# Optimization experiments

Hardware: AMD Instinct MI355X
Metric: run time of the kernel (lower is better)

## Reference

```python
import jax, jax.numpy as jnp
import numpy as np

N = 100000
EPS = 1e-5

def gcn_conv(x, W, b, src, dst, n):
    # linear transform first (PyG GCNConv): [N, H]
    h = x @ W
    # add self-loops
    loop = jnp.arange(n, dtype=src.dtype)
    s = jnp.concatenate([src, loop])
    d = jnp.concatenate([dst, loop])
    # symmetric normalization deg^{-1/2}[s] * deg^{-1/2}[d]
    deg = jax.ops.segment_sum(jnp.ones_like(d, dtype=h.dtype), d, num_segments=n)
    dinv = jnp.where(deg > 0, jax.lax.rsqrt(jnp.maximum(deg, 1.0) * 0 + jnp.where(deg > 0, deg, 1.0)), 0.0)
    norm = dinv[s] * dinv[d]
    msg = h[s] * norm[:, None]          # gather + scale: [E+N, H]
    out = jax.ops.segment_sum(msg, d, num_segments=n)  # scatter-add
    return out + b

def batch_norm(x, gamma, beta):
    mu = jnp.mean(x, axis=0)
    var = jnp.mean((x - mu) ** 2, axis=0)  # biased var, as BatchNorm1d training
    return (x - mu) * jax.lax.rsqrt(var + EPS) * gamma + beta

def setup_inputs() -> dict:
    key = jax.random.key(0)
    ks = jax.random.split(key, 8)
    D, H, O = 64, 64, 32
    E = 1600000
    x = jax.random.normal(ks[0], (N, D), dtype=jnp.float32)
    edge_index = jax.random.randint(ks[1], (2, E), 0, N, dtype=jnp.int64)
    W1 = jax.random.normal(ks[2], (D, H), dtype=jnp.float32) / np.sqrt(D)
    b1 = jnp.zeros((H,), dtype=jnp.float32)
    W2 = jax.random.normal(ks[3], (H, H), dtype=jnp.float32) / np.sqrt(H)
    b2 = jnp.zeros((H,), dtype=jnp.float32)
    gamma1 = jnp.ones((H,), dtype=jnp.float32); beta1 = jnp.zeros((H,), dtype=jnp.float32)
    gamma2 = jnp.ones((H,), dtype=jnp.float32); beta2 = jnp.zeros((H,), dtype=jnp.float32)
    Wfc = jax.random.normal(ks[4], (H, O), dtype=jnp.float32) / np.sqrt(H)
    bfc = jnp.zeros((O,), dtype=jnp.float32)
    return {"x": x, "edge_index": edge_index, "W1": W1, "b1": b1, "gamma1": gamma1, "beta1": beta1,
            "W2": W2, "b2": b2, "gamma2": gamma2, "beta2": beta2, "Wfc": Wfc, "bfc": bfc}

def reference(x, edge_index, W1, b1, gamma1, beta1, W2, b2, gamma2, beta2, Wfc, bfc):
    src, dst = edge_index[0], edge_index[1]
    h = jax.nn.relu(gcn_conv(x, W1, b1, src, dst, N))
    h = batch_norm(h, gamma1, beta1)
    h = jax.nn.relu(gcn_conv(h, W2, b2, src, dst, N))
    h = batch_norm(h, gamma2, beta2)
    return h @ Wfc + bfc
```

## Files before the change

kernel.cpp:

```cpp
#include <hip/hip_runtime.h>
#include <hip/hip_bf16.h>
#include <cstdint>
#include <cstddef>

#define NBK 128
#define BKB 512

static __device__ __forceinline__ unsigned pack_bf16(float a, float b) {
  __hip_bfloat16 lo = __float2bfloat16(a), hi = __float2bfloat16(b);
  unsigned short ulo = *reinterpret_cast<unsigned short*>(&lo);
  unsigned short uhi = *reinterpret_cast<unsigned short*>(&hi);
  return ((unsigned)uhi << 16) | ulo;
}
static __device__ __forceinline__ float blo(unsigned u) {
  union { unsigned q; float f; } x; x.q = u << 16; return x.f;
}
static __device__ __forceinline__ float bhi(unsigned u) {
  union { unsigned q; float f; } x; x.q = u & 0xffff0000u; return x.f;
}


__launch_bounds__(256)
__global__ void bucket_kernel(const int* __restrict__ src, const int* __restrict__ dst,
                              int E, int cap, int nbk,
                              int* __restrict__ bcur, int* __restrict__ rcnt,
                              int* __restrict__ bkt_d, int* __restrict__ bkt_s) {
  __shared__ int cnt[NBK], base[NBK], gbase[NBK], curb[NBK], pbase[NBK];
  __shared__ int ptot_s;
  __shared__ int stg_d[3200], stg_s[3200];
  int t = threadIdx.x;
  int chunk = (E + BKB - 1) / BKB;
  int ebeg = blockIdx.x * chunk;
  int eend = min(E, ebeg + chunk);
  int nloc = eend - ebeg;
  for (int q = t; q < nbk; q += 256) { cnt[q] = 0; curb[q] = 0; }
  __syncthreads();

  int dl[13], sl[13];
  int nr = (nloc + 255) >> 8;
#pragma unroll 13
  for (int u = 0; u < nr; ++u) {
    int li = (u << 8) + t;
    bool v = li < nloc;
    int i = ebeg + (v ? li : 0);
    int d = v ? __builtin_nontemporal_load(&dst[i]) : 0;
    int s = v ? __builtin_nontemporal_load(&src[i]) : 0;
    dl[u] = d; sl[u] = s;
    if (v) atomicAdd(&cnt[d >> 10], 1);
  }
  __syncthreads();
  if (t == 0) {
    int run = 0, prun = 0;
    for (int q = 0; q < nbk; ++q) {
      base[q] = run;  run += cnt[q];
      pbase[q] = prun; prun += (cnt[q] + 15) & ~15;
    }
    ptot_s = prun;
  }
  __syncthreads();
  for (int q = t; q < nbk; q += 256) {
    int c = cnt[q];
    if (c > 0) {
      gbase[q] = atomicAdd(&bcur[q], (c + 15) & ~15);
      atomicAdd(&rcnt[q], c);
    } else gbase[q] = 0;
  }
#pragma unroll 13
  for (int u = 0; u < nr; ++u) {
    int li = (u << 8) + t;
    if (li < nloc) {
      int b = dl[u] >> 10;
      int pos = atomicAdd(&curb[b], 1) + base[b];
      stg_d[pos] = dl[u]; stg_s[pos] = sl[u];
    }
  }
  __syncthreads();
  int ptot = ptot_s;
  for (int i = t; i < ptot; i += 256) {
    int lo = 0, hi = nbk - 1;
    while (lo < hi) {
      int mid = (lo + hi + 1) >> 1;
      if (pbase[mid] <= i) lo = mid; else hi = mid - 1;
    }
    int q = lo;
    int j = i - pbase[q];
    int dv = -1, sv = 0;
    if (j < cnt[q]) { dv = stg_d[base[q] + j]; sv = stg_s[base[q] + j]; }
    size_t o = (size_t)q * cap + gbase[q] + j;
    bkt_d[o] = dv;
    bkt_s[o] = sv;
  }
}

__global__ void bscan_kernel(const int* __restrict__ rcnt, int nbk, int* __restrict__ bbase,
                             int E, int n, int* __restrict__ rowptr) {
  __shared__ int sm[NBK];
  int t = threadIdx.x;
  int v = (t < nbk) ? rcnt[t] : 0;
  sm[t] = v;
  __syncthreads();
  for (int off = 1; off < NBK; off <<= 1) {
    int x = (t >= off) ? sm[t - off] : 0;
    __syncthreads();
    sm[t] += x;
    __syncthreads();
  }
  if (t < nbk) bbase[t] = sm[t] - v;
  if (t == 0) rowptr[n] = E;
}

__launch_bounds__(1024)
__global__ void scatter2_kernel(const int* __restrict__ bkt_d, const int* __restrict__ bkt_s,
                                const int* __restrict__ bcur, const int* __restrict__ bbase,
                                int cap, int n,
                                int* __restrict__ rowptr, float* __restrict__ dinv,
                                int* __restrict__ adj) {
  __shared__ int hist[1024];
  __shared__ int cur[1024];
  int b = blockIdx.x;
  int nodebase = b << 10;
  int nn = min(1024, n - nodebase);
  int t = threadIdx.x;
  hist[t] = 0;
  __syncthreads();

  int cnt = bcur[b];
  const int* bd = bkt_d + (size_t)b * cap;
  const int* bs = bkt_s + (size_t)b * cap;

  for (int i = t; i < cnt; i += 1024) {
    int d = bd[i];
    if (d >= 0) atomicAdd(&hist[d - nodebase], 1);
  }
  __syncthreads();

  int deg = hist[t];
  int v = deg;
  cur[t] = v;
  __syncthreads();
  for (int off = 1; off < 1024; off <<= 1) {
    int x = (t >= off) ? cur[t - off] : 0;
    __syncthreads();
    cur[t] += x;
    __syncthreads();
  }
  int excl = cur[t] - v;
  int gb = bbase[b];
  if (t < nn) {
    rowptr[nodebase + t] = gb + excl;
    dinv[nodebase + t] = rsqrtf((float)(deg + 1));
  }
  __syncthreads();
  cur[t] = gb + excl;
  __syncthreads();

  for (int i = t; i < cnt; i += 1024) {
    int d = bd[i];
    if (d >= 0) {
      int s = bs[i];
      int pos = atomicAdd(&cur[d - nodebase], 1);
      adj[pos] = s;
    }
  }
}


template <int OUT, bool BF16OUT, bool BN, bool ABF16>
__launch_bounds__(256)
__global__ void gemm_kernel(const void* __restrict__ Ap, const float* __restrict__ W,
                            const float* __restrict__ bnacc,
                            const float* __restrict__ gamma, const float* __restrict__ beta,
                            const float* __restrict__ bias, const float* __restrict__ rowscale,
                            void* __restrict__ Cout, int n, float invn) {
  constexpr int OQ = OUT / 4;
  __shared__ float lds[64 * 65];
  __shared__ float sc_s[64], sh_s[64];
  int t = threadIdx.x;
  int row0 = blockIdx.x * 64;
  int rows = n - row0; if (rows > 64) rows = 64;

  if (BN) {
    if (t < 64) {
      float su = 0.f, sq = 0.f;
#pragma unroll
      for (int c = 0; c < 8; ++c) {
        su += bnacc[c * 128 + t];
        sq += bnacc[c * 128 + 64 + t];
      }
      float mu = su * invn;
      float var = sq * invn - mu * mu;
      float sc = gamma[t] * rsqrtf(var + 1e-5f);
      sc_s[t] = sc;
      sh_s[t] = fmaf(-mu, sc, beta[t]);
    }
    __syncthreads();
  }

  if (ABF16) {
    const uint4* A4 = (const uint4*)((const unsigned short*)Ap + (size_t)row0 * 64);
#pragma unroll
    for (int j = 0; j < 2; ++j) {
      int idx = t + j * 256;
      int r = idx >> 3, c8 = idx & 7;
      uint4 v = make_uint4(0, 0, 0, 0);
      if (r < rows) v = A4[idx];
      float f[8] = {blo(v.x), bhi(v.x), blo(v.y), bhi(v.y),
                    blo(v.z), bhi(v.z), blo(v.w), bhi(v.w)};
      float* p = &lds[r * 65 + c8 * 8];
#pragma unroll
      for (int q = 0; q < 8; ++q) {
        float xv = f[q];
        if (BN) xv = fmaf(xv, sc_s[c8 * 8 + q], sh_s[c8 * 8 + q]);
        p[q] = xv;
      }
    }
  } else {
    const float4* A4 = (const float4*)((const float*)Ap + (size_t)row0 * 64);
#pragma unroll
    for (int j = 0; j < 4; ++j) {
      int idx = t + j * 256;
      int r = idx >> 4, c4 = idx & 15;
      float4 v = make_float4(0.f, 0.f, 0.f, 0.f);
      if (r < rows) v = A4[idx];
      if (BN) {
        int c = c4 * 4;
        v.x = fmaf(v.x, sc_s[c + 0], sh_s[c + 0]);
        v.y = fmaf(v.y, sc_s[c + 1], sh_s[c + 1]);
        v.z = fmaf(v.z, sc_s[c + 2], sh_s[c + 2]);
        v.w = fmaf(v.w, sc_s[c + 3], sh_s[c + 3]);
      }
      float* p = &lds[r * 65 + c4 * 4];
      p[0] = v.x; p[1] = v.y; p[2] = v.z; p[3] = v.w;
    }
  }
  __syncthreads();

  const int w = __builtin_amdgcn_readfirstlane(t >> 6);
  const int r = t & 63;
  float acc[OQ];
#pragma unroll
  for (int o = 0; o < OQ; ++o) acc[o] = 0.f;
  const float* Ar = &lds[r * 65];
  const float* Wp = W + w * OQ;
  for (int k = 0; k < 64; ++k) {
    float a = Ar[k];
#pragma unroll
    for (int o = 0; o < OQ; ++o) acc[o] = fmaf(a, Wp[k * OUT + o], acc[o]);
  }
  if (rowscale) {
    int rr = row0 + r; if (rr >= n) rr = n - 1;
    float rs = rowscale[rr];
#pragma unroll
    for (int o = 0; o < OQ; ++o) acc[o] *= rs;
  }
  if (bias) {
    const float* Bp = bias + w * OQ;
#pragma unroll
    for (int o = 0; o < OQ; ++o) acc[o] += Bp[o];
  }

  if (r < rows) {
    if (BF16OUT) {
      unsigned pk[OQ / 2];
#pragma unroll
      for (int o2 = 0; o2 < OQ / 2; ++o2) pk[o2] = pack_bf16(acc[2 * o2], acc[2 * o2 + 1]);
      uint4* cp = (uint4*)((__hip_bfloat16*)Cout + (size_t)(row0 + r) * OUT + w * OQ);
#pragma unroll
      for (int j = 0; j < OQ / 8; ++j) {
        uint4 v; v.x = pk[j * 4]; v.y = pk[j * 4 + 1]; v.z = pk[j * 4 + 2]; v.w = pk[j * 4 + 3];
        cp[j] = v;
      }
    } else {
      float4* cp = (float4*)((float*)Cout + (size_t)(row0 + r) * OUT + w * OQ);
#pragma unroll
      for (int j = 0; j < OQ / 4; ++j)
        cp[j] = make_float4(acc[j * 4], acc[j * 4 + 1], acc[j * 4 + 2], acc[j * 4 + 3]);
    }
  }
}


__launch_bounds__(256, 8)
__global__ void agg_kernel(const __hip_bfloat16* __restrict__ g, const int* __restrict__ rowptr,
                           const int* __restrict__ adj, const float* __restrict__ dinv,
                           const float* __restrict__ bias, __hip_bfloat16* __restrict__ out,
                           float* __restrict__ bnacc, int n) {
  const int tid = threadIdx.x;
  const int lane = tid & 63;
  const int wave = tid >> 6;
  const int grp = lane >> 3;
  const int sub = lane & 7;
  const int gw = blockIdx.x * 4 + wave;

  const unsigned short* gu = (const unsigned short*)g;

  int d = gw * 8 + grp;
  int beg = rowptr[d];
  int k = rowptr[d + 1] - beg;
  float di = dinv[d];

  const uint4 v0 = *(const uint4*)(gu + (((size_t)d) << 6) + sub * 8);
  float acc[8];
  acc[0] = blo(v0.x); acc[1] = bhi(v0.x);
  acc[2] = blo(v0.y); acc[3] = bhi(v0.y);
  acc[4] = blo(v0.z); acc[5] = bhi(v0.z);
  acc[6] = blo(v0.w); acc[7] = bhi(v0.w);

  int kmax = k;
  kmax = max(kmax, __shfl_xor(kmax, 8));
  kmax = max(kmax, __shfl_xor(kmax, 16));
  kmax = max(kmax, __shfl_xor(kmax, 32));

  for (int j0 = 0; j0 < kmax; j0 += 8) {
    uint4 vv[8];
    float w[8];
#pragma unroll
    for (int u = 0; u < 8; ++u) {
      int idx = j0 + u;
      int aoff = (idx < k) ? idx : 0;
      int s = __builtin_nontemporal_load(&adj[beg + aoff]);
      unsigned su = ((unsigned)s < (unsigned)n) ? (unsigned)s : (unsigned)d;
      vv[u] = *(const uint4*)(gu + (((size_t)su) << 6) + sub * 8);
      w[u] = (idx < k) ? 1.f : 0.f;
    }
#pragma unroll
    for (int u = 0; u < 8; ++u) {
      acc[0] = fmaf(w[u], blo(vv[u].x), acc[0]);
      acc[1] = fmaf(w[u], bhi(vv[u].x), acc[1]);
      acc[2] = fmaf(w[u], blo(vv[u].y), acc[2]);
      acc[3] = fmaf(w[u], bhi(vv[u].y), acc[3]);
      acc[4] = fmaf(w[u], blo(vv[u].z), acc[4]);
      acc[5] = fmaf(w[u], bhi(vv[u].z), acc[5]);
      acc[6] = fmaf(w[u], blo(vv[u].w), acc[6]);
      acc[7] = fmaf(w[u], bhi(vv[u].w), acc[7]);
    }
  }

  float bias8[8];
  {
    const float4* bp = (const float4*)(bias + sub * 8);
    float4 b0 = bp[0], b1 = bp[1];
    bias8[0]=b0.x; bias8[1]=b0.y; bias8[2]=b0.z; bias8[3]=b0.w;
    bias8[4]=b1.x; bias8[5]=b1.y; bias8[6]=b1.z; bias8[7]=b1.w;
  }

  float o[8], s1[8], s2[8];
#pragma unroll
  for (int j = 0; j < 8; ++j) {
    float v = fmaf(acc[j], di, bias8[j]);
    v = fmaxf(v, 0.f);
    o[j] = v;
    s1[j] = v;
    s2[j] = v * v;
  }
  uint4 ov;
  ov.x = pack_bf16(o[0], o[1]); ov.y = pack_bf16(o[2], o[3]);
  ov.z = pack_bf16(o[4], o[5]); ov.w = pack_bf16(o[6], o[7]);
  *(uint4*)((unsigned short*)out + (((size_t)d) << 6) + sub * 8) = ov;

#pragma unroll
  for (int j = 0; j < 8; ++j) {
    s1[j] += __shfl_xor(s1[j], 8);  s2[j] += __shfl_xor(s2[j], 8);
    s1[j] += __shfl_xor(s1[j], 16); s2[j] += __shfl_xor(s2[j], 16);
    s1[j] += __shfl_xor(s1[j], 32); s2[j] += __shfl_xor(s2[j], 32);
  }
  __shared__ float redA[4][64], redB[4][64];
  if (lane < 8) {
#pragma unroll
    for (int j = 0; j < 8; ++j) {
      redA[wave][sub * 8 + j] = s1[j];
      redB[wave][sub * 8 + j] = s2[j];
    }
  }
  __syncthreads();
  if (tid < 64) {
    float a = redA[0][tid] + redA[1][tid] + redA[2][tid] + redA[3][tid];
    float b = redB[0][tid] + redB[1][tid] + redB[2][tid] + redB[3][tid];
    float* dst = bnacc + (blockIdx.x & 7) * 128;
    atomicAdd(&dst[tid], a);
    atomicAdd(&dst[64 + tid], b);
  }
}


extern "C" void kernel_launch(void* const* d_in, const int* in_sizes, int n_in,
                              void* d_out, int out_size, void* d_ws, size_t ws_size,
                              hipStream_t stream) {
  const float* x      = (const float*)d_in[0];
  const int*   ei     = (const int*)d_in[1];
  const float* W1     = (const float*)d_in[2];
  const float* b1     = (const float*)d_in[3];
  const float* gamma1 = (const float*)d_in[4];
  const float* beta1  = (const float*)d_in[5];
  const float* W2     = (const float*)d_in[6];
  const float* b2     = (const float*)d_in[7];
  const float* gamma2 = (const float*)d_in[8];
  const float* beta2  = (const float*)d_in[9];
  const float* Wfc    = (const float*)d_in[10];
  const float* bfc    = (const float*)d_in[11];

  int n = in_sizes[0] / 64;
  int E = in_sizes[1] / 2;
  const int* src = ei;
  const int* dst = ei + E;

  char* base = (char*)d_ws;
  size_t off = 0;
  auto alloc = [&](size_t bytes) -> char* {
    char* p = base + off;
    off += (bytes + 255) & ~(size_t)255;
    return p;
  };
  int*   rowptr = (int*)alloc((size_t)(n + 1) * 4);
  int*   adj    = (int*)alloc(((size_t)E + 64) * 4);
  float* dinv   = (float*)alloc((size_t)n * 4);
  float* bn     = (float*)alloc(2048 * 4);
  int*   bcur   = (int*)alloc(NBK * 4);
  int*   rcnt   = (int*)alloc(NBK * 4);
  int*   bbase  = (int*)alloc(NBK * 4);
  __hip_bfloat16* hbuf = (__hip_bfloat16*)alloc((size_t)n * 64 * 2);
  char*  rraw   = alloc((size_t)n * 64 * 4);
  __hip_bfloat16* rbuf = (__hip_bfloat16*)rraw;
  int nbk = (n + 1023) >> 10;
  int cap = 24576;
  int* bkt_d = (int*)rraw;
  int* bkt_s = bkt_d + (size_t)nbk * cap;
  (void)ws_size; (void)n_in; (void)out_size;

  hipMemsetAsync(bn, 0, 2048 * 4, stream);
  hipMemsetAsync(bcur, 0, NBK * 4, stream);
  hipMemsetAsync(rcnt, 0, NBK * 4, stream);

  bucket_kernel<<<BKB, 256, 0, stream>>>(src, dst, E, cap, nbk, bcur, rcnt, bkt_d, bkt_s);
  bscan_kernel<<<1, NBK, 0, stream>>>(rcnt, nbk, bbase, E, n, rowptr);
  scatter2_kernel<<<nbk, 1024, 0, stream>>>(bkt_d, bkt_s, bcur, bbase, cap, n,
                                            rowptr, dinv, adj);

  int gg = (n + 63) / 64;
  int ga = n / 32;
  float invn = 1.0f / (float)n;
  gemm_kernel<64, true, false, false><<<gg, 256, 0, stream>>>(
      x, W1, nullptr, nullptr, nullptr, nullptr, dinv, hbuf, n, 0.f);
  agg_kernel<<<ga, 256, 0, stream>>>(hbuf, rowptr, adj, dinv, b1, rbuf, bn, n);
  gemm_kernel<64, true, true, true><<<gg, 256, 0, stream>>>(
      rbuf, W2, bn, gamma1, beta1, nullptr, dinv, hbuf, n, invn);
  agg_kernel<<<ga, 256, 0, stream>>>(hbuf, rowptr, adj, dinv, b2, rbuf, bn + 1024, n);
  gemm_kernel<32, false, true, true><<<gg, 256, 0, stream>>>(
      rbuf, Wfc, bn + 1024, gamma2, beta2, bfc, nullptr, d_out, n, invn);
}
```

Baseline: 281.5 us.

## Degree-sort nodes per bucket for balanced aggregation; fold bucket scan into scatter

After: 314.1 us. 1.12x slower.

```diff
diff --git a/kernel.cpp b/kernel.cpp
--- a/kernel.cpp
+++ b/kernel.cpp
@@ -92,37 +92,31 @@
   }
 }
 
-__global__ void bscan_kernel(const int* __restrict__ rcnt, int nbk, int* __restrict__ bbase,
-                             int E, int n, int* __restrict__ rowptr) {
-  __shared__ int sm[NBK];
-  int t = threadIdx.x;
-  int v = (t < nbk) ? rcnt[t] : 0;
-  sm[t] = v;
-  __syncthreads();
-  for (int off = 1; off < NBK; off <<= 1) {
-    int x = (t >= off) ? sm[t - off] : 0;
-    __syncthreads();
-    sm[t] += x;
-    __syncthreads();
-  }
-  if (t < nbk) bbase[t] = sm[t] - v;
-  if (t == 0) rowptr[n] = E;
-}
-
 __launch_bounds__(1024)
 __global__ void scatter2_kernel(const int* __restrict__ bkt_d, const int* __restrict__ bkt_s,
-                                const int* __restrict__ bcur, const int* __restrict__ bbase,
-                                int cap, int n,
+                                const int* __restrict__ bcur, const int* __restrict__ rcnt,
+                                int cap, int n, int nbk,
                                 int* __restrict__ rowptr, float* __restrict__ dinv,
-                                int* __restrict__ adj) {
+                                unsigned* __restrict__ perm, int* __restrict__ adj) {
   __shared__ int hist[1024];
   __shared__ int cur[1024];
+  __shared__ int sbb[NBK];
+  __shared__ int bins[64], bincur[64];
   int b = blockIdx.x;
   int nodebase = b << 10;
   int nn = min(1024, n - nodebase);
   int t = threadIdx.x;
   hist[t] = 0;
-  __syncthreads();
+  if (t < NBK) sbb[t] = (t < nbk) ? rcnt[t] : 0;
+  if (t < 64) bins[t] = 0;
+  __syncthreads();
+  for (int off = 1; off < NBK; off <<= 1) {
+    int x = (t >= off && t < NBK) ? sbb[t - off] : 0;
+    __syncthreads();
+    if (t < NBK) sbb[t] += x;
+    __syncthreads();
+  }
+  int gb = (b > 0) ? sbb[b - 1] : 0;
 
   int cnt = bcur[b];
   const int* bd = bkt_d + (size_t)b * cap;
@@ -145,10 +139,27 @@
     __syncthreads();
   }
   int excl = cur[t] - v;
-  int gb = bbase[b];
   if (t < nn) {
     rowptr[nodebase + t] = gb + excl;
     dinv[nodebase + t] = rsqrtf((float)(deg + 1));
+  }
+
+  int mybin = min(deg, 63);
+  if (t < nn) atomicAdd(&bins[mybin], 1);
+  __syncthreads();
+  if (t < 64) bincur[t] = bins[t];
+  __syncthreads();
+  for (int off = 1; off < 64; off <<= 1) {
+    int x = (t >= off && t < 64) ? bincur[t - off] : 0;
+    __syncthreads();
+    if (t < 64) bincur[t] += x;
+    __syncthreads();
+  }
+  if (t < 64) bincur[t] -= bins[t];
+  __syncthreads();
+  if (t < nn) {
+    int rank = atomicAdd(&bincur[mybin], 1);
+    perm[nodebase + rank] = (unsigned)(nodebase + t) | ((unsigned)deg << 20);
   }
   __syncthreads();
   cur[t] = gb + excl;
@@ -283,6 +294,7 @@
 __launch_bounds__(256, 8)
 __global__ void agg_kernel(const __hip_bfloat16* __restrict__ g, const int* __restrict__ rowptr,
                            const int* __restrict__ adj, const float* __restrict__ dinv,
+                           const unsigned* __restrict__ perm,
                            const float* __restrict__ bias, __hip_bfloat16* __restrict__ out,
                            float* __restrict__ bnacc, int n) {
   const int tid = threadIdx.x;
@@ -294,9 +306,10 @@
 
   const unsigned short* gu = (const unsigned short*)g;
 
-  int d = gw * 8 + grp;
+  const unsigned pe = perm[gw * 8 + grp];
+  const int d = (int)(pe & 0xFFFFFu);
+  const int k = (int)(pe >> 20);
   int beg = rowptr[d];
-  int k = rowptr[d + 1] - beg;
   float di = dinv[d];
 
   const uint4 v0 = *(const uint4*)(gu + (((size_t)d) << 6) + sub * 8);
@@ -414,10 +427,10 @@
   int*   rowptr = (int*)alloc((size_t)(n + 1) * 4);
   int*   adj    = (int*)alloc(((size_t)E + 64) * 4);
   float* dinv   = (float*)alloc((size_t)n * 4);
+  unsigned* perm = (unsigned*)alloc((size_t)n * 4);
   float* bn     = (float*)alloc(2048 * 4);
   int*   bcur   = (int*)alloc(NBK * 4);
   int*   rcnt   = (int*)alloc(NBK * 4);
-  int*   bbase  = (int*)alloc(NBK * 4);
   __hip_bfloat16* hbuf = (__hip_bfloat16*)alloc((size_t)n * 64 * 2);
   char*  rraw   = alloc((size_t)n * 64 * 4);
   __hip_bfloat16* rbuf = (__hip_bfloat16*)rraw;
@@ -427,24 +440,21 @@
   int* bkt_s = bkt_d + (size_t)nbk * cap;
   (void)ws_size; (void)n_in; (void)out_size;
 
-  hipMemsetAsync(bn, 0, 2048 * 4, stream);
-  hipMemsetAsync(bcur, 0, NBK * 4, stream);
-  hipMemsetAsync(rcnt, 0, NBK * 4, stream);
+  hipMemsetAsync(bn, 0, 2048 * 4 + NBK * 4 + NBK * 4, stream);
 
   bucket_kernel<<<BKB, 256, 0, stream>>>(src, dst, E, cap, nbk, bcur, rcnt, bkt_d, bkt_s);
-  bscan_kernel<<<1, NBK, 0, stream>>>(rcnt, nbk, bbase, E, n, rowptr);
-  scatter2_kernel<<<nbk, 1024, 0, stream>>>(bkt_d, bkt_s, bcur, bbase, cap, n,
-                                            rowptr, dinv, adj);
+  scatter2_kernel<<<nbk, 1024, 0, stream>>>(bkt_d, bkt_s, bcur, rcnt, cap, n, nbk,
+                                            rowptr, dinv, perm, adj);
 
   int gg = (n + 63) / 64;
   int ga = n / 32;
   float invn = 1.0f / (float)n;
   gemm_kernel<64, true, false, false><<<gg, 256, 0, stream>>>(
       x, W1, nullptr, nullptr, nullptr, nullptr, dinv, hbuf, n, 0.f);
-  agg_kernel<<<ga, 256, 0, stream>>>(hbuf, rowptr, adj, dinv, b1, rbuf, bn, n);
+  agg_kernel<<<ga, 256, 0, stream>>>(hbuf, rowptr, adj, dinv, perm, b1, rbuf, bn, n);
   gemm_kernel<64, true, true, true><<<gg, 256, 0, stream>>>(
       rbuf, W2, bn, gamma1, beta1, nullptr, dinv, hbuf, n, invn);
-  agg_kernel<<<ga, 256, 0, stream>>>(hbuf, rowptr, adj, dinv, b2, rbuf, bn + 1024, n);
+  agg_kernel<<<ga, 256, 0, stream>>>(hbuf, rowptr, adj, dinv, perm, b2, rbuf, bn + 1024, n);
   gemm_kernel<32, false, true, true><<<gg, 256, 0, stream>>>(
       rbuf, Wfc, bn + 1024, gamma2, beta2, bfc, nullptr, d_out, n, invn);
 }
```
